# Kernel tuning notes

Hardware: AMD Instinct MI355X
Metric: run time of the kernel (lower is better)

## Reference

```python
import jax, jax.numpy as jnp
import numpy as np
from jax import lax

N_SIN = 3

def _bn(x, g, b, m, v, eps):
    sh = [1] * x.ndim; sh[1] = -1
    r = lambda t: t.reshape(sh)
    return (x - r(m)) / jnp.sqrt(r(v) + eps) * r(g) + r(b)

def _conv2d(x, w, b, padding):
    y = lax.conv_general_dilated(x, w, (1, 1), padding,
                                 dimension_numbers=('NCHW', 'OIHW', 'NCHW'))
    return y + b[None, :, None, None]

def _causal_conv1d(x, w, b):
    k = w.shape[-1]
    y = lax.conv_general_dilated(x, w, (1,), [(k - 1, 0)],
                                 dimension_numbers=('NCH', 'OIH', 'NCH'))
    return y + b[None, :, None]

def _se(x, w1, w2):
    y = x.mean(axis=2)                                   # [B,C] global avg pool
    y = jax.nn.sigmoid(jax.nn.relu(y @ w1.T) @ w2.T)
    return x * y[:, :, None]

def _kan(x, W1, W2, B1, B2):
    # x: [B,din]; per-edge tiny MLP: sin/cos embed -> linear -> silu -> linear
    omega = (2.0 ** jnp.arange(N_SIN)).astype(x.dtype)   # [n_sin]
    ox = x[..., None] * omega                            # [B,din,n_sin]
    feat = jnp.concatenate([x[..., None], jnp.sin(ox), jnp.cos(ox)], axis=-1)  # [B,din,7]
    h = jnp.einsum('bif,ijhf->bijh', feat, W1) + B1[None]  # [B,din,dout,h]
    h = jax.nn.silu(h)
    out = jnp.einsum('bijh,ijh->bij', h, W2[:, :, 0, :]) + B2[None, :, :, 0]
    return out.sum(axis=1)                               # [B,dout]

def _lstm(x, w_ih, w_hh, b_ih, b_hh):
    B, T, E = x.shape
    H = w_hh.shape[1]
    def step(carry, xt):
        h, c = carry
        g = xt @ w_ih.T + h @ w_hh.T + (b_ih + b_hh)
        i, f, gg, o = jnp.split(g, 4, axis=-1)           # torch gate order i,f,g,o
        c = jax.nn.sigmoid(f) * c + jax.nn.sigmoid(i) * jnp.tanh(gg)
        h = jax.nn.sigmoid(o) * jnp.tanh(c)
        return (h, c), h
    init = (jnp.zeros((B, H), x.dtype), jnp.zeros((B, H), x.dtype))
    _, hs = lax.scan(step, init, jnp.swapaxes(x, 0, 1))
    return jnp.swapaxes(hs, 0, 1)                        # [B,T,H]

def _cluster(hidden):
    B, T, H = hidden.shape
    last = hidden[:, -1, :]
    hn = hidden / jnp.maximum(jnp.linalg.norm(hidden, axis=-1, keepdims=True), 1e-8)
    sim = jnp.einsum('bth,bsh->bts', hn, hn)
    sim = jnp.exp(-5.5 * (1.0 - sim))
    sim = sim * (1.0 - jnp.eye(T, dtype=sim.dtype))      # zero diagonal
    # 2-D prefix sums replace the O(T) python loop over block means
    S = jnp.cumsum(jnp.cumsum(sim, axis=1), axis=2)
    Sii = jnp.diagonal(S, axis1=1, axis2=2)[:, :T - 1]   # sum of [:i,:i]
    R = S[:, -1, :T - 1]                                 # sum of [:, :i]
    C = S[:, :T - 1, -1]                                 # sum of [:i, :]
    tot = S[:, -1, -1][:, None]
    i_f = jnp.arange(1, T, dtype=sim.dtype)
    dist = (Sii / i_f**2
            + (tot - R - C + Sii) / (T - i_f)**2
            - (C - Sii) / (i_f * (T - i_f))
            - (R - Sii) / (i_f * (T - i_f)))             # [B,T-1]
    cuts = jnp.argmax(dist, axis=1) + 1                  # [B]
    mask = (jnp.arange(T)[None, :] < cuts[:, None]).astype(hidden.dtype)
    corr = (hidden * mask[:, :, None]).sum(axis=1) / cuts[:, None].astype(hidden.dtype)
    return last, corr

def reference(x, we1, be1, bn_e1_g, bn_e1_b, bn_e1_m, bn_e1_v, we2, be2, bn_e2_g, bn_e2_b, bn_e2_m, bn_e2_v, w_ih, w_hh, b_ih, b_hh, mu_W1, mu_W2, mu_B1, mu_B2, std_W1, std_W2, std_B1, std_B2, muc_W1, muc_W2, muc_B1, muc_B2, stdc_W1, stdc_W2, stdc_B1, stdc_B2, fc_W1, fc_W2, fc_B1, fc_B2, wc1, bc1, bn1_g, bn1_b, bn1_m, bn1_v, se1_w1, se1_w2, wc2, bc2, bn2_g, bn2_b, bn2_m, bn2_v, se2_w1, se2_w2, wc3, bc3, bn3_g, bn3_b, bn3_m, bn3_v, eps1, eps2):
    gelu = lambda t: jax.nn.gelu(t, approximate=False)
    x = jnp.transpose(x, (0, 2, 1))                      # shuffle: [B,T,F]->[B,F,T]
    h2d = _conv2d(x[:, None], we1, be1, 'SAME')          # [B,4E,F,T]
    h2d = gelu(_bn(h2d, bn_e1_g, bn_e1_b, bn_e1_m, bn_e1_v, 1e-5))
    h2d = _conv2d(h2d, we2, be2, 'VALID')                # [B,E,1,T]
    h2d = gelu(_bn(h2d, bn_e2_g, bn_e2_b, bn_e2_m, bn_e2_v, 1e-5))
    x_src = jnp.transpose(h2d[:, :, 0, :], (0, 2, 1))    # [B,T,E]
    hseq = _lstm(x_src, w_ih, w_hh, b_ih, b_hh)          # [B,T,H]
    out, corr = _cluster(hseq)
    mu = _kan(corr, mu_W1, mu_W2, mu_B1, mu_B2)
    std = jax.nn.softplus(_kan(corr, std_W1, std_W2, std_B1, std_B2) - 5.0)
    z = mu + std * eps1
    x_z = jnp.concatenate([out, z], axis=1)              # [B,2H]
    mu_c = _kan(x_z, muc_W1, muc_W2, muc_B1, muc_B2)
    std_c = jax.nn.softplus(_kan(x_z, stdc_W1, stdc_W2, stdc_B1, stdc_B2) - 5.0)
    x1 = mu_c + std_c * eps2                             # dropout = identity (eval)
    x2 = jnp.transpose(x, (0, 2, 1))                     # [B,T,F]: channels = seq_len
    x2 = gelu(_bn(_causal_conv1d(x2, wc1, bc1), bn1_g, bn1_b, bn1_m, bn1_v, 1e-3))
    x2 = _se(x2, se1_w1, se1_w2)
    x2 = gelu(_bn(_causal_conv1d(x2, wc2, bc2), bn2_g, bn2_b, bn2_m, bn2_v, 1e-3))
    x2 = _se(x2, se2_w1, se2_w2)
    x2 = gelu(_bn(_causal_conv1d(x2, wc3, bc3), bn3_g, bn3_b, bn3_m, bn3_v, 1e-3))
    x2 = x2.mean(axis=2)                                 # [B,conv3_nf]
    x_all = jnp.concatenate([x1, x2], axis=1)            # [B, H+conv3_nf]
    return _kan(x_all, fc_W1, fc_W2, fc_B1, fc_B2)       # [B,num_classes]

def setup_inputs():
    key = jax.random.key(0)
    ks = iter(jax.random.split(key, 128))
    f32 = jnp.float32
    def n(shape, s=0.05):
        return s * jax.random.normal(next(ks), shape, f32)
    def bn_params(c):
        g = 1.0 + 0.05 * jax.random.normal(next(ks), (c,), f32)
        b = 0.05 * jax.random.normal(next(ks), (c,), f32)
        m = 0.05 * jax.random.normal(next(ks), (c,), f32)
        v = jax.random.uniform(next(ks), (c,), f32, 0.5, 1.5)
        return g, b, m, v
    def kan_params(din, dout, h=32, feat=1 + 2 * N_SIN):
        s = (2.0 / (feat + h)) ** 0.5
        return (n((din, dout, h, feat), s), n((din, dout, 1, h), s),
                jnp.zeros((din, dout, h), f32), jnp.zeros((din, dout, 1), f32))
    B, T, F_, E, H = 32, 256, 32, 64, 128
    inp = {}
    inp['x'] = jax.random.normal(next(ks), (B, T, F_), f32)
    inp['we1'] = n((4 * E, 1, 1, 8)); inp['be1'] = n((4 * E,))
    inp['bn_e1_g'], inp['bn_e1_b'], inp['bn_e1_m'], inp['bn_e1_v'] = bn_params(4 * E)
    inp['we2'] = n((E, 4 * E, F_, 1)); inp['be2'] = n((E,))
    inp['bn_e2_g'], inp['bn_e2_b'], inp['bn_e2_m'], inp['bn_e2_v'] = bn_params(E)
    inp['w_ih'] = n((4 * H, E)); inp['w_hh'] = n((4 * H, H))
    inp['b_ih'] = n((4 * H,)); inp['b_hh'] = n((4 * H,))
    for nm, (di, do) in [('mu', (H, H)), ('std', (H, H)), ('muc', (2 * H, H)), ('stdc', (2 * H, H)), ('fc', (2 * H, 10))]:
        w1, w2, b1, b2 = kan_params(di, do)
        inp[nm + '_W1'], inp[nm + '_W2'], inp[nm + '_B1'], inp[nm + '_B2'] = w1, w2, b1, b2
    inp['wc1'] = n((128, T, 8)); inp['bc1'] = n((128,))
    inp['bn1_g'], inp['bn1_b'], inp['bn1_m'], inp['bn1_v'] = bn_params(128)
    inp['se1_w1'] = n((8, 128)); inp['se1_w2'] = n((128, 8))
    inp['wc2'] = n((256, 128, 5)); inp['bc2'] = n((256,))
    inp['bn2_g'], inp['bn2_b'], inp['bn2_m'], inp['bn2_v'] = bn_params(256)
    inp['se2_w1'] = n((16, 256)); inp['se2_w2'] = n((256, 16))
    inp['wc3'] = n((128, 256, 3)); inp['bc3'] = n((128,))
    inp['bn3_g'], inp['bn3_b'], inp['bn3_m'], inp['bn3_v'] = bn_params(128)
    inp['eps1'] = jax.random.normal(next(ks), (B, H), f32)
    inp['eps2'] = jax.random.normal(next(ks), (B, H), f32)
    return inp
```

## Files before the change

### kernel.cpp

```cpp
#include <hip/hip_runtime.h>
#include <hip/hip_bf16.h>
#include <math.h>

typedef __hip_bfloat16 bf16;

#define DEV static __device__ __forceinline__

DEV float geluf(float x){ return 0.5f*x*(1.0f + erff(x*0.70710678118654752f)); }
DEV float sigmf(float x){ return 1.0f/(1.0f + __expf(-x)); }
DEV float softplusf(float x){ return (x > 15.f) ? x : log1pf(__expf(x)); }
DEV float tanhfast(float x){ float e = __expf(2.f*x); return fmaf(-2.f, 1.f/(e+1.f), 1.f); }

typedef __attribute__((ext_vector_type(8))) short v8s;
typedef __attribute__((ext_vector_type(4))) float v4f;
typedef _Float16 f16;
typedef f16 h2 __attribute__((ext_vector_type(2)));
typedef f16 f16x8 __attribute__((ext_vector_type(8)));
typedef unsigned u32x4 __attribute__((ext_vector_type(4)));

DEV float dot2f(h2 a, h2 b, float c){
#if __has_builtin(__builtin_amdgcn_fdot2)
  return __builtin_amdgcn_fdot2(a, b, c, false);
#else
  return fmaf((float)a.y, (float)b.y, fmaf((float)a.x, (float)b.x, c));
#endif
}

DEV h2 geth2(f16x8 v, int j){ h2 r; r.x = v[2*j]; r.y = v[2*j+1]; return r; }

DEV void lds_barrier(){
  asm volatile("s_waitcnt lgkmcnt(0)" ::: "memory");
  __builtin_amdgcn_s_barrier();
  __builtin_amdgcn_sched_barrier(0);
}

enum : size_t {
  OFF_W1F   = 0,
  OFF_B1F   = 2048,
  OFF_S2E   = 2304,
  OFF_B2E   = 2368,
  OFF_WIHT  = 2432,
  OFF_BIASG = 35200,
  OFF_WHHT  = 35712,
  OFF_EPI1S = 101248,
  OFF_EPI1B = 101376,
  OFF_EPI2S = 101504,
  OFF_EPI2B = 101760,
  OFF_EPI3S = 102016,
  OFF_EPI3B = 102144,
  OFF_WE2B  = 102272,
  OFF_XSRC  = 364416,
  OFF_GX    = 888704,
  OFF_HSEQ  = 5083008,
  OFF_HN    = 6131584,
  OFF_PCOL  = 7180160,
  OFF_CCOL  = 7188352,
  OFF_CUTS  = 7196544,
  OFF_LAST  = 7196576,
  OFF_CORR  = 7200672,
  OFF_FEATA = 7204768,
  OFF_MUO   = 7233440,
  OFF_STDO  = 7237536,
  OFF_XZ    = 7241632,
  OFF_FEATB = 7249824,
  OFF_MUCO  = 7307168,
  OFF_STDCO = 7311264,
  OFF_XC1   = 7315360,
  OFF_XC2   = 7446432,
  OFF_KP    = 7708576,
  OFF_B2S   = 7741344,
  OFF_X2F   = 7839648,
  OFF_XALL  = 7843744,
  OFF_FEATC = 7851936,
  WS_FLOATS = 7909280
};

__global__ __launch_bounds__(256) void prep_kernel(
    const float* we1, const float* be1,
    const float* e1g, const float* e1b, const float* e1m, const float* e1v,
    const float* we2, const float* be2, const float* e2g, const float* e2b, const float* e2m, const float* e2v,
    const float* wih, const float* whh, const float* bih, const float* bhh,
    const float* bc1, const float* c1g, const float* c1b, const float* c1m, const float* c1v,
    const float* bc2, const float* c2g, const float* c2b, const float* c2m, const float* c2v,
    const float* bc3, const float* c3g, const float* c3b, const float* c3m, const float* c3v,
    const float* muB2, const float* sdB2, const float* mcB2, const float* scB2, const float* fcB2,
    float* ws)
{
  int idx = blockIdx.x*256 + threadIdx.x;
  if(idx < 2048){
    int o = idx>>3;
    float s = e1g[o] * rsqrtf(e1v[o] + 1e-5f);
    ws[OFF_W1F + idx] = we1[idx] * s;
  } else if(idx < 2304){
    int o = idx - 2048;
    float s = e1g[o] * rsqrtf(e1v[o] + 1e-5f);
    ws[OFF_B1F + o] = s*(be1[o] - e1m[o]) + e1b[o];
  } else if(idx < 2368){
    int e = idx - 2304;
    float s = e2g[e] * rsqrtf(e2v[e] + 1e-5f);
    ws[OFF_S2E + e] = s;
    ws[OFF_B2E + e] = s*(be2[e] - e2m[e]) + e2b[e];
  } else if(idx < 35136){
    int q = idx - 2368; int e = q>>9, g = q&511;
    ws[OFF_WIHT + q] = wih[g*64 + e];
  } else if(idx < 35648){
    int g = idx - 35136;
    ws[OFF_BIASG + g] = bih[g] + bhh[g];
  } else if(idx < 101184){
    int q = idx - 35648;
    if(q < 32768){
      int k2 = q>>9, g = q&511;
      h2 v;
      v.x = (f16)whh[g*128 + 2*k2];
      v.y = (f16)whh[g*128 + 2*k2 + 1];
      ((h2*)(ws + OFF_WHHT))[g*64 + k2] = v;
    }
  } else if(idx < 101312){
    int o = idx - 101184;
    float s = c1g[o] * rsqrtf(c1v[o] + 1e-3f);
    ws[OFF_EPI1S + o] = s;
    ws[OFF_EPI1B + o] = s*(bc1[o] - c1m[o]) + c1b[o];
  } else if(idx < 101568){
    int o = idx - 101312;
    float s = c2g[o] * rsqrtf(c2v[o] + 1e-3f);
    ws[OFF_EPI2S + o] = s;
    ws[OFF_EPI2B + o] = s*(bc2[o] - c2m[o]) + c2b[o];
  } else if(idx < 101696){
    int o = idx - 101568;
    float s = c3g[o] * rsqrtf(c3v[o] + 1e-3f);
    ws[OFF_EPI3S + o] = s;
    ws[OFF_EPI3B + o] = s*(bc3[o] - c3m[o]) + c3b[o];
  } else if(idx < 625984){
    int q = idx - 101696;
    int o = q >> 11, rem = q & 2047;
    int e = rem >> 5, f = rem & 31;
    bf16* Wr = (bf16*)(ws + OFF_WE2B);
    Wr[q] = __float2bfloat16(we2[(size_t)e*8192 + o*32 + f]);
  } else if(idx < 626112){
    int j = idx - 625984; float s = 0.f;
    for(int i=0;i<128;i++) s += muB2[i*128+j];
    ws[OFF_B2S + j] = s;
  } else if(idx < 626240){
    int j = idx - 626112; float s = 0.f;
    for(int i=0;i<128;i++) s += sdB2[i*128+j];
    ws[OFF_B2S + 128 + j] = s;
  } else if(idx < 626368){
    int j = idx - 626240; float s = 0.f;
    for(int i=0;i<256;i++) s += mcB2[i*128+j];
    ws[OFF_B2S + 256 + j] = s;
  } else if(idx < 626496){
    int j = idx - 626368; float s = 0.f;
    for(int i=0;i<256;i++) s += scB2[i*128+j];
    ws[OFF_B2S + 384 + j] = s;
  } else if(idx < 626506){
    int j = idx - 626496; float s = 0.f;
    for(int i=0;i<256;i++) s += fcB2[i*10+j];
    ws[OFF_B2S + 512 + j] = s;
  }
}

__global__ __launch_bounds__(256,1) void encoder_kernel(
    const float* __restrict__ x, const float* __restrict__ w1f, const float* __restrict__ b1f,
    const float* __restrict__ s2e, const float* __restrict__ b2e,
    const bf16* __restrict__ Wr, float* __restrict__ x_src)
{
  __shared__ float xs[39*32];
  __shared__ float w1s[2048];
  __shared__ float b1s[256];
  __shared__ __align__(16) unsigned short At[2][32*136];
  __shared__ __align__(16) unsigned short Bt[2][4*2560];

  int blk = blockIdx.x; int b = blk>>3; int t0 = (blk&7)*32;
  int tid = threadIdx.x;

  for(int i=tid;i<2048;i+=256) w1s[i] = w1f[i];
  b1s[tid] = b1f[tid];
  for(int i=tid;i<39*32;i+=256){
    int r=i>>5, f=i&31; int t=t0-3+r;
    xs[i] = (t>=0 && t<256) ? x[(b*256+t)*32+f] : 0.f;
  }
  __syncthreads();

  int f = tid & 31, tq = tid >> 5;
  int lane = tid & 63, w = tid >> 6;
  int wm = w & 1, wn = w >> 1;
  int m0 = wm*16, n0 = wn*32;
  int l15 = lane & 15, quad = lane >> 4;

  const v8s* Wv = (const v8s*)Wr;

  auto stage = [&](int cc, int buf){
    v8s bw[4];
    #pragma unroll
    for(int i=0;i<4;i++) bw[i] = Wv[cc*1024 + i*256 + tid];
    unsigned short aval[16];
    #pragma unroll
    for(int ol=0;ol<4;ol++){
      int o = cc*4 + ol;
      float wv[8];
      #pragma unroll
      for(int j=0;j<8;j++) wv[j] = w1s[o*8+j];
      float bb = b1s[o];
      #pragma unroll
      for(int i=0;i<4;i++){
        int tl = tq*4 + i;
        float c = bb;
        #pragma unroll
        for(int j=0;j<8;j++) c = fmaf(wv[j], xs[(tl+j)*32+f], c);
        aval[ol*4+i] = ((__hip_bfloat16_raw)__float2bfloat16(geluf(c))).x;
      }
    }
    #pragma unroll
    for(int ol=0;ol<4;ol++){
      #pragma unroll
      for(int i=0;i<4;i++)
        At[buf][(tq*4+i)*136 + ol*32 + f] = aval[ol*4+i];
    }
    #pragma unroll
    for(int i=0;i<4;i++){
      int j = i*256 + tid;
      int ol = j>>8, e = (j&255)>>2, f8 = j&3;
      *(v8s*)&Bt[buf][ol*2560 + e*40 + f8*8] = bw[i];
    }
  };

  stage(0, 0);
  __syncthreads();

  v4f acc0 = {0.f,0.f,0.f,0.f}, acc1 = {0.f,0.f,0.f,0.f};

  for(int c=0;c<64;c++){
    int p = c & 1, q = p ^ 1;
    if(c < 63) stage(c+1, q);
    #pragma unroll
    for(int ol=0;ol<4;ol++){
      v8s av = *(const v8s*)&At[p][(m0+l15)*136 + ol*32 + quad*8];
      v8s b0 = *(const v8s*)&Bt[p][ol*2560 + (n0+l15)*40 + quad*8];
      v8s b1 = *(const v8s*)&Bt[p][ol*2560 + (n0+16+l15)*40 + quad*8];
      acc0 = __builtin_amdgcn_mfma_f32_16x16x32_bf16(av, b0, acc0, 0, 0, 0);
      acc1 = __builtin_amdgcn_mfma_f32_16x16x32_bf16(av, b1, acc1, 0, 0, 0);
    }
    __syncthreads();
  }

  #pragma unroll
  for(int r=0;r<4;r++){
    int t = t0 + m0 + quad*4 + r;
    int e0 = n0 + l15;
    float v0 = geluf(s2e[e0]*acc0[r] + b2e[e0]);
    x_src[((size_t)(b*256+t))*64 + e0] = v0;
    int e1 = e0 + 16;
    float v1 = geluf(s2e[e1]*acc1[r] + b2e[e1]);
    x_src[((size_t)(b*256+t))*64 + e1] = v1;
  }
}

__global__ __launch_bounds__(256) void gates_kernel(
    const float* x_src, const float* wihT, const float* biasg, float* gx)
{
  __shared__ float xsh[32*64];
  int blk = blockIdx.x; int b = blk>>3, t0 = (blk&7)*32;
  int tid = threadIdx.x;
  for(int i=tid;i<2048;i+=256) xsh[i] = x_src[((size_t)b*256+t0)*64 + i];
  __syncthreads();
  int g0 = tid, g1 = tid + 256;
  float acc0[32], acc1[32];
  #pragma unroll
  for(int tt=0;tt<32;tt++){ acc0[tt]=0.f; acc1[tt]=0.f; }
  for(int e=0;e<64;e++){
    float w0 = wihT[e*512+g0], w1 = wihT[e*512+g1];
    #pragma unroll
    for(int tt=0;tt<32;tt++){
      float xv = xsh[tt*64+e];
      acc0[tt] = fmaf(xv, w0, acc0[tt]);
      acc1[tt] = fmaf(xv, w1, acc1[tt]);
    }
  }
  float bg0 = biasg[g0], bg1 = biasg[g1];
  #pragma unroll
  for(int tt=0;tt<32;tt++){
    gx[((size_t)b*256+t0+tt)*512 + g0] = acc0[tt] + bg0;
    gx[((size_t)b*256+t0+tt)*512 + g1] = acc1[tt] + bg1;
  }
}

#define LSTM_STEP(AG, BG, PR, PW, T)                                         \
  {                                                                          \
    const f16x8* hp = (const f16x8*)&hsh[PR][half*64];                       \
    f16x8 hvv[8];                                                            \
    _Pragma("unroll")                                                        \
    for(int q=0;q<8;q++) hvv[q] = hp[q];                                     \
    float sA0=0.f,sA1=0.f,sB0=0.f,sB1=0.f;                                   \
    _Pragma("unroll")                                                        \
    for(int q=0;q<8;q++){                                                    \
      f16x8 W8a = __builtin_bit_cast(f16x8, wa[q]);                          \
      f16x8 W8b = __builtin_bit_cast(f16x8, wb[q]);                          \
      f16x8 hq = hvv[q];                                                     \
      sA0 = dot2f(geth2(hq,0), geth2(W8a,0), sA0);                           \
      sA1 = dot2f(geth2(hq,1), geth2(W8a,1), sA1);                           \
      sA0 = dot2f(geth2(hq,2), geth2(W8a,2), sA0);                           \
      sA1 = dot2f(geth2(hq,3), geth2(W8a,3), sA1);                           \
      sB0 = dot2f(geth2(hq,0), geth2(W8b,0), sB0);                           \
      sB1 = dot2f(geth2(hq,1), geth2(W8b,1), sB1);                           \
      sB0 = dot2f(geth2(hq,2), geth2(W8b,2), sB0);                           \
      sB1 = dot2f(geth2(hq,3), geth2(W8b,3), sB1);                           \
    }                                                                        \
    float pA = sA0+sA1, pB = sB0+sB1;                                        \
    float fullA = (AG) + pA + __shfl_xor(pA, 32, 64);                        \
    float fullB = (BG) + pB + __shfl_xor(pB, 32, 64);                        \
    float argA = dup ? 2.f*fullA : -fullA;                                   \
    float eA = __expf(argA);                                                 \
    float qA = 1.f/(eA + 1.f);                                               \
    float vA = dup ? fmaf(-2.f, qA, 1.f) : qA;      \
    float vB = 1.f/(1.f + __expf(-fullB));          \
    float oA = __shfl_xor(vA, 16, 64);                                       \
    float oB = __shfl_xor(vB, 16, 64);                                       \
    float iv = dup ? oA : vA;                                                \
    float gv = dup ? vA : oA;                                                \
    float fv = dup ? oB : vB;                                                \
    float ov = dup ? vB : oB;                                                \
    c = fmaf(fv, c, iv*gv);                                                  \
    float h = ov*tanhfast(c);                                                \
    if(lane < 16){                                                           \
      hsh[PW][n] = (f16)h;                                                   \
      hseq[((size_t)b*256+(T))*128 + n] = h;                                 \
    }                                                                        \
    lds_barrier();                                                           \
  }

__global__ __launch_bounds__(512)
__attribute__((amdgpu_waves_per_eu(2,2)))
void lstm_kernel(
    const float* __restrict__ gates_x, const float* __restrict__ whh16f, float* __restrict__ hseq)
{
  __shared__ __align__(16) f16 hsh[2][128];
  int b = blockIdx.x, tt = threadIdx.x;
  int wave = tt >> 6, lane = tt & 63;
  int n = wave*16 + (lane & 15);
  int dup  = (lane >> 4) & 1;
  int half = lane >> 5;
  int gA = dup ? (256 + n) : n;
  int gB = gA + 128;

  const u32x4* Wp = (const u32x4*)whh16f;
  u32x4 wa[8], wb[8];
  #pragma unroll
  for(int q=0;q<8;q++){
    wa[q] = Wp[gA*16 + half*8 + q];
    wb[q] = Wp[gB*16 + half*8 + q];
  }
  asm volatile("" :
    "+v"(wa[0]), "+v"(wa[1]), "+v"(wa[2]), "+v"(wa[3]),
    "+v"(wa[4]), "+v"(wa[5]), "+v"(wa[6]), "+v"(wa[7]),
    "+v"(wb[0]), "+v"(wb[1]), "+v"(wb[2]), "+v"(wb[3]),
    "+v"(wb[4]), "+v"(wb[5]), "+v"(wb[6]), "+v"(wb[7]));

  if(tt < 128) hsh[0][tt] = (f16)0.f;
  float c = 0.f;
  const float* gx = gates_x + (size_t)b*256*512;
  float aC = gx[gA],       bC = gx[gB];
  float aN = gx[512 + gA], bN = gx[512 + gB];
  __syncthreads();
  for(int t=0; t<256; t+=2){
    float a2=0.f, b2=0.f, a3=0.f, b3=0.f;
    if(t+2 < 256){ a2 = gx[(size_t)(t+2)*512 + gA]; b2 = gx[(size_t)(t+2)*512 + gB]; }
    LSTM_STEP(aC, bC, 0, 1, t);
    if(t+3 < 256){ a3 = gx[(size_t)(t+3)*512 + gA]; b3 = gx[(size_t)(t+3)*512 + gB]; }
    LSTM_STEP(aN, bN, 1, 0, t+1);
    aC=a2; bC=b2; aN=a3; bN=b3;
  }
}

__global__ __launch_bounds__(64) void hn_kernel(const float* hseq, float* hn)
{
  size_t row = blockIdx.x; int lane = threadIdx.x;
  const float* hp = hseq + row*128;
  float v0 = hp[lane], v1 = hp[lane+64];
  float ss = v0*v0 + v1*v1;
  #pragma unroll
  for(int m=1;m<64;m<<=1) ss += __shfl_xor(ss, m, 64);
  float r = 1.f / fmaxf(sqrtf(ss), 1e-8f);
  hn[row*128 + lane]      = v0*r;
  hn[row*128 + 64 + lane] = v1*r;
}

__global__ __launch_bounds__(256) void pc_kernel(const float* hn, float* pcol, float* ccol)
{
  int blk = blockIdx.x; int b = blk>>3, chunk = blk&7;
  int tid = threadIdx.x; int il = tid & 31, ts = tid >> 5;
  int i = chunk*32 + il;
  const float4* hb = (const float4*)(hn + (size_t)b*32768);
  float4 hi[32];
  #pragma unroll
  for(int r=0;r<32;r++) hi[r] = hb[(size_t)i*32 + r];
  float ps=0.f, cs=0.f;
  for(int t=ts*32; t<ts*32+32; t++){
    float dx=0.f, dy=0.f, dz=0.f, dw=0.f;
    #pragma unroll
    for(int r=0;r<32;r++){
      float4 hv = hb[(size_t)t*32 + r];
      dx = fmaf(hi[r].x, hv.x, dx);
      dy = fmaf(hi[r].y, hv.y, dy);
      dz = fmaf(hi[r].z, hv.z, dz);
      dw = fmaf(hi[r].w, hv.w, dw);
    }
    float dot = (dx+dy)+(dz+dw);
    float sim = (t==i) ? 0.f : expf(-5.5f*(1.0f - dot));
    cs += sim;
    if(t < i) ps += sim;
  }
  __shared__ float red[16][32];
  red[ts][il] = ps; red[8+ts][il] = cs;
  __syncthreads();
  if(tid < 32){
    float s=0.f;
    for(int r=0;r<8;r++) s += red[r][tid];
    pcol[b*256 + chunk*32 + tid] = s;
  } else if(tid < 64){
    int c2 = tid - 32; float s=0.f;
    for(int r=0;r<8;r++) s += red[8+r][c2];
    ccol[b*256 + chunk*32 + c2] = s;
  }
}

__global__ __launch_bounds__(256) void cutcorr_kernel(
    const float* pcol, const float* ccol, const float* hseq,
    float* last, float* corr, int* cuts)
{
  int b = blockIdx.x, tid = threadIdx.x;
  __shared__ float D[256], RC[256], dist[256];
  __shared__ int cutsh;
  if(tid == 0){
    float d=0.f, r=0.f;
    for(int i=0;i<256;i++){
      d += 2.f*pcol[b*256+i]; D[i]=d;
      r += ccol[b*256+i];     RC[i]=r;
    }
  }
  __syncthreads();
  float tot = RC[255];
  if(tid < 255){
    float Dv = D[tid], Rv = RC[tid];
    float i_f = (float)(tid+1), j_f = 256.f - i_f;
    dist[tid] = Dv/(i_f*i_f) + (tot - 2.f*Rv + Dv)/(j_f*j_f) - 2.f*(Rv - Dv)/(i_f*j_f);
  }
  __syncthreads();
  if(tid == 0){
    float best = dist[0]; int bi = 0;
    for(int i=1;i<255;i++) if(dist[i] > best){ best = dist[i]; bi = i; }
    cutsh = bi + 1; cuts[b] = cutsh;
  }
  __syncthreads();
  int cut = cutsh;
  int k = tid & 127, half = tid >> 7;
  float s = 0.f;
  for(int t=half; t<cut; t+=2) s += hseq[((size_t)b*256+t)*128 + k];
  __shared__ float partial[2][128];
  partial[half][k] = s;
  __syncthreads();
  if(tid < 128){
    corr[b*128+tid] = (partial[0][tid] + partial[1][tid]) / (float)cut;
    last[b*128+tid] = hseq[((size_t)b*256+255)*128 + tid];
  }
}

__global__ __launch_bounds__(256) void feat_kernel(const float* xin, float* feat, int n)
{
  int idx = blockIdx.x*256 + threadIdx.x;
  if(idx >= n) return;
  float xv = xin[idx];
  float* fp = feat + (size_t)idx*7;
  fp[0]=xv;
  fp[1]=sinf(xv); fp[2]=sinf(2.f*xv); fp[3]=sinf(4.f*xv);
  fp[4]=cosf(xv); fp[5]=cosf(2.f*xv); fp[6]=cosf(4.f*xv);
}

__global__ __launch_bounds__(256) void kanp_kernel(
    const float* __restrict__ feat, const float* __restrict__ W1,
    const float* __restrict__ B1, const float* __restrict__ W2,
    int din, int dout, float* __restrict__ partial)
{
  __shared__ float feat_s[32*225];
  __shared__ float red[8][32];
  int j = blockIdx.x, ic = blockIdx.y;
  int i0 = ic*32;
  int tid = threadIdx.x;
  int b = tid & 31, hg = tid >> 5;
  for(int q=tid; q<1792; q+=256){
    int br = q/56, qq = q - br*56;
    float4 v = *(const float4*)(feat + ((size_t)br*din + i0)*7 + qq*4);
    float* d = &feat_s[br*225 + qq*4];
    d[0]=v.x; d[1]=v.y; d[2]=v.z; d[3]=v.w;
  }
  __syncthreads();
  float acc = 0.f;
  const float* fb = &feat_s[b*225];
  for(int ii=0; ii<32; ii++){
    int i = i0 + ii;
    size_t hbase = ((size_t)i*dout + j)*32 + hg*4;
    const float4* w1p = (const float4*)(W1 + ((size_t)i*dout + j)*224 + hg*28);
    float w1a[28];
    #pragma unroll
    for(int q=0;q<7;q++) *(float4*)&w1a[q*4] = w1p[q];
    float4 b1v = *(const float4*)(B1 + hbase);
    float4 w2v = *(const float4*)(W2 + hbase);
    float f[7];
    #pragma unroll
    for(int q=0;q<7;q++) f[q] = fb[ii*7+q];
    float b1a[4] = {b1v.x, b1v.y, b1v.z, b1v.w};
    float w2a[4] = {w2v.x, w2v.y, w2v.z, w2v.w};
    #pragma unroll
    for(int hh=0;hh<4;hh++){
      float hv = b1a[hh];
      #pragma unroll
      for(int q=0;q<7;q++) hv = fmaf(f[q], w1a[hh*7+q], hv);
      float sv = hv / (1.f + __expf(-hv));
      acc = fmaf(sv, w2a[hh], acc);
    }
  }
  red[hg][b] = acc;
  __syncthreads();
  if(tid < 32){
    float s = 0.f;
    #pragma unroll
    for(int q=0;q<8;q++) s += red[q][tid];
    partial[((size_t)ic*32 + tid)*dout + j] = s;
  }
}

__global__ __launch_bounds__(256) void kanr_kernel(
    const float* __restrict__ partial, const float* __restrict__ b2s,
    int NI, int dout, float* __restrict__ outp)
{
  int idx = blockIdx.x*256 + threadIdx.x;
  if(idx >= 32*dout) return;
  int b = idx / dout, j = idx - b*dout;
  float s = b2s[j];
  for(int ic=0; ic<NI; ic++) s += partial[((size_t)ic*32 + b)*dout + j];
  outp[idx] = s;
}

__global__ __launch_bounds__(256) void zmix_kernel(
    const float* muo, const float* stdo, const float* eps1, const float* last, float* xz)
{
  int idx = blockIdx.x*256 + threadIdx.x;
  if(idx >= 4096) return;
  int b = idx >> 7, k = idx & 127;
  float z = muo[idx] + softplusf(stdo[idx] - 5.f)*eps1[idx];
  xz[b*256 + k]       = last[idx];
  xz[b*256 + 128 + k] = z;
}

__global__ __launch_bounds__(256) void xall_kernel(
    const float* muco, const float* stdco, const float* eps2, const float* x2f, float* xa)
{
  int idx = blockIdx.x*256 + threadIdx.x;
  if(idx >= 4096) return;
  int b = idx >> 7, k = idx & 127;
  xa[b*256 + k]       = muco[idx] + softplusf(stdco[idx] - 5.f)*eps2[idx];
  xa[b*256 + 128 + k] = x2f[idx];
}

template<int CIN, int K, int COUT, int NCH, int LG>
__global__ __launch_bounds__(COUT*LG, 1) void convp_kernel(
    const float* __restrict__ xin, const float* __restrict__ w, float* __restrict__ part)
{
  constexpr int L = 32/LG;
  constexpr int CCH = CIN/NCH;
  __shared__ float xsh[CCH*32];
  int b = blockIdx.x, ch = blockIdx.y;
  int tid = threadIdx.x;
  for(int i=tid; i<CCH*32; i+=COUT*LG) xsh[i] = xin[((size_t)b*CIN + ch*CCH)*32 + i];
  __syncthreads();
  int o = tid / LG, lh = tid % LG;
  int l0 = lh*L;
  float acc[L];
  #pragma unroll
  for(int j=0;j<L;j++) acc[j]=0.f;
  const float* wrow = w + ((size_t)o*CIN + ch*CCH)*K;
  for(int c=0;c<CCH;c++){
    float wv[K];
    #pragma unroll
    for(int k=0;k<K;k++) wv[k] = wrow[c*K + k];
    float xr[L+K-1];
    #pragma unroll
    for(int i=0;i<L+K-1;i++){
      int li = l0 - (K-1) + i;
      xr[i] = (li>=0) ? xsh[c*32+li] : 0.f;
    }
    #pragma unroll
    for(int j=0;j<L;j++){
      #pragma unroll
      for(int k=0;k<K;k++) acc[j] = fmaf(xr[j+k], wv[k], acc[j]);
    }
  }
  float* pp = part + (((size_t)ch*32 + b)*COUT + o)*32 + l0;
  #pragma unroll
  for(int j=0;j<L;j++) pp[j] = acc[j];
}

template<int C, int R, int NP>
__global__ __launch_bounds__(C,1) void sef_kernel(
    const float* __restrict__ part, const float* __restrict__ epi_s, const float* __restrict__ epi_b,
    const float* __restrict__ w1, const float* __restrict__ w2, float* __restrict__ out)
{
  __shared__ float mean[C];
  __shared__ float y1[R];
  int b = blockIdx.x, c = threadIdx.x;
  float g[32];
  #pragma unroll
  for(int l=0;l<32;l++) g[l]=0.f;
  for(int p=0;p<NP;p++){
    const float* pp = part + (((size_t)p*32 + b)*C + c)*32;
    #pragma unroll
    for(int l=0;l<32;l++) g[l] += pp[l];
  }
  float s = epi_s[c], bb = epi_b[c];
  float m = 0.f;
  #pragma unroll
  for(int l=0;l<32;l++){ g[l] = geluf(s*g[l]+bb); m += g[l]; }
  mean[c] = m*(1.f/32.f);
  __syncthreads();
  if(c < R){
    float t=0.f;
    for(int k=0;k<C;k++) t = fmaf(mean[k], w1[c*C+k], t);
    y1[c] = fmaxf(t,0.f);
  }
  __syncthreads();
  float t=0.f;
  #pragma unroll
  for(int k=0;k<R;k++) t = fmaf(y1[k], w2[c*R+k], t);
  float sc = sigmf(t);
  float* op = out + ((size_t)b*C + c)*32;
  #pragma unroll
  for(int l=0;l<32;l++) op[l] = g[l]*sc;
}

__global__ __launch_bounds__(128,1) void mean3f_kernel(
    const float* __restrict__ part, const float* __restrict__ epi_s, const float* __restrict__ epi_b,
    float* __restrict__ x2f)
{
  int b = blockIdx.x, c = threadIdx.x;
  float g[32];
  #pragma unroll
  for(int l=0;l<32;l++) g[l]=0.f;
  for(int p=0;p<8;p++){
    const float* pp = part + (((size_t)p*32 + b)*128 + c)*32;
    #pragma unroll
    for(int l=0;l<32;l++) g[l] += pp[l];
  }
  float s = epi_s[c], bb = epi_b[c];
  float m = 0.f;
  #pragma unroll
  for(int l=0;l<32;l++) m += geluf(s*g[l]+bb);
  x2f[b*128 + c] = m*(1.f/32.f);
}

extern "C" void kernel_launch(void* const* d_in, const int* in_sizes, int n_in,
                              void* d_out, int out_size, void* d_ws, size_t ws_size,
                              hipStream_t stream)
{
  const float* x    = (const float*)d_in[0];
  const float* we1  = (const float*)d_in[1];
  const float* be1  = (const float*)d_in[2];
  const float* e1g  = (const float*)d_in[3];
  const float* e1b  = (const float*)d_in[4];
  const float* e1m  = (const float*)d_in[5];
  const float* e1v  = (const float*)d_in[6];
  const float* we2  = (const float*)d_in[7];
  const float* be2  = (const float*)d_in[8];
  const float* e2g  = (const float*)d_in[9];
  const float* e2b  = (const float*)d_in[10];
  const float* e2m  = (const float*)d_in[11];
  const float* e2v  = (const float*)d_in[12];
  const float* wih  = (const float*)d_in[13];
  const float* whh  = (const float*)d_in[14];
  const float* bih  = (const float*)d_in[15];
  const float* bhh  = (const float*)d_in[16];
  const float* muW1 = (const float*)d_in[17];
  const float* muW2 = (const float*)d_in[18];
  const float* muB1 = (const float*)d_in[19];
  const float* muB2 = (const float*)d_in[20];
  const float* sdW1 = (const float*)d_in[21];
  const float* sdW2 = (const float*)d_in[22];
  const float* sdB1 = (const float*)d_in[23];
  const float* sdB2 = (const float*)d_in[24];
  const float* mcW1 = (const float*)d_in[25];
  const float* mcW2 = (const float*)d_in[26];
  const float* mcB1 = (const float*)d_in[27];
  const float* mcB2 = (const float*)d_in[28];
  const float* scW1 = (const float*)d_in[29];
  const float* scW2 = (const float*)d_in[30];
  const float* scB1 = (const float*)d_in[31];
  const float* scB2 = (const float*)d_in[32];
  const float* fcW1 = (const float*)d_in[33];
  const float* fcW2 = (const float*)d_in[34];
  const float* fcB1 = (const float*)d_in[35];
  const float* fcB2 = (const float*)d_in[36];
  const float* wc1  = (const float*)d_in[37];
  const float* bc1  = (const float*)d_in[38];
  const float* c1g  = (const float*)d_in[39];
  const float* c1b  = (const float*)d_in[40];
  const float* c1m  = (const float*)d_in[41];
  const float* c1v  = (const float*)d_in[42];
  const float* se1w1= (const float*)d_in[43];
  const float* se1w2= (const float*)d_in[44];
  const float* wc2  = (const float*)d_in[45];
  const float* bc2  = (const float*)d_in[46];
  const float* c2g  = (const float*)d_in[47];
  const float* c2b  = (const float*)d_in[48];
  const float* c2m  = (const float*)d_in[49];
  const float* c2v  = (const float*)d_in[50];
  const float* se2w1= (const float*)d_in[51];
  const float* se2w2= (const float*)d_in[52];
  const float* wc3  = (const float*)d_in[53];
  const float* bc3  = (const float*)d_in[54];
  const float* c3g  = (const float*)d_in[55];
  const float* c3b  = (const float*)d_in[56];
  const float* c3m  = (const float*)d_in[57];
  const float* c3v  = (const float*)d_in[58];
  const float* eps1 = (const float*)d_in[59];
  const float* eps2 = (const float*)d_in[60];

  float* ws = (float*)d_ws;
  float* part = ws + OFF_GX;
  float* kp   = ws + OFF_KP;
  float* b2s  = ws + OFF_B2S;

  prep_kernel<<<2448, 256, 0, stream>>>(we1, be1, e1g,e1b,e1m,e1v,
      we2, be2,e2g,e2b,e2m,e2v, wih,whh,bih,bhh,
      bc1,c1g,c1b,c1m,c1v, bc2,c2g,c2b,c2m,c2v, bc3,c3g,c3b,c3m,c3v,
      muB2, sdB2, mcB2, scB2, fcB2, ws);

  encoder_kernel<<<256, 256, 0, stream>>>(x, ws+OFF_W1F, ws+OFF_B1F,
      ws+OFF_S2E, ws+OFF_B2E, (const bf16*)(ws+OFF_WE2B), ws+OFF_XSRC);

  gates_kernel<<<256, 256, 0, stream>>>(ws+OFF_XSRC, ws+OFF_WIHT, ws+OFF_BIASG, ws+OFF_GX);
  lstm_kernel<<<32, 512, 0, stream>>>(ws+OFF_GX, ws+OFF_WHHT, ws+OFF_HSEQ);

  hn_kernel<<<8192, 64, 0, stream>>>(ws+OFF_HSEQ, ws+OFF_HN);
  pc_kernel<<<256, 256, 0, stream>>>(ws+OFF_HN, ws+OFF_PCOL, ws+OFF_CCOL);
  cutcorr_kernel<<<32, 256, 0, stream>>>(ws+OFF_PCOL, ws+OFF_CCOL, ws+OFF_HSEQ,
      ws+OFF_LAST, ws+OFF_CORR, (int*)(ws+OFF_CUTS));

  feat_kernel<<<16, 256, 0, stream>>>(ws+OFF_CORR, ws+OFF_FEATA, 4096);
  kanp_kernel<<<dim3(128,4), 256, 0, stream>>>(ws+OFF_FEATA, muW1, muB1, muW2, 128, 128, kp);
  kanr_kernel<<<16, 256, 0, stream>>>(kp, b2s+0, 4, 128, ws+OFF_MUO);
  kanp_kernel<<<dim3(128,4), 256, 0, stream>>>(ws+OFF_FEATA, sdW1, sdB1, sdW2, 128, 128, kp);
  kanr_kernel<<<16, 256, 0, stream>>>(kp, b2s+128, 4, 128, ws+OFF_STDO);
  zmix_kernel<<<16, 256, 0, stream>>>(ws+OFF_MUO, ws+OFF_STDO, eps1, ws+OFF_LAST, ws+OFF_XZ);
  feat_kernel<<<32, 256, 0, stream>>>(ws+OFF_XZ, ws+OFF_FEATB, 8192);
  kanp_kernel<<<dim3(128,8), 256, 0, stream>>>(ws+OFF_FEATB, mcW1, mcB1, mcW2, 256, 128, kp);
  kanr_kernel<<<16, 256, 0, stream>>>(kp, b2s+256, 8, 128, ws+OFF_MUCO);
  kanp_kernel<<<dim3(128,8), 256, 0, stream>>>(ws+OFF_FEATB, scW1, scB1, scW2, 256, 128, kp);
  kanr_kernel<<<16, 256, 0, stream>>>(kp, b2s+384, 8, 128, ws+OFF_STDCO);

  convp_kernel<256,8,128,8,2><<<dim3(32,8), 256, 0, stream>>>(x, wc1, part);
  sef_kernel<128,8,8><<<32, 128, 0, stream>>>(part, ws+OFF_EPI1S, ws+OFF_EPI1B, se1w1, se1w2, ws+OFF_XC1);
  convp_kernel<128,5,256,4,1><<<dim3(32,4), 256, 0, stream>>>(ws+OFF_XC1, wc2, part);
  sef_kernel<256,16,4><<<32, 256, 0, stream>>>(part, ws+OFF_EPI2S, ws+OFF_EPI2B, se2w1, se2w2, ws+OFF_XC2);
  convp_kernel<256,3,128,8,2><<<dim3(32,8), 256, 0, stream>>>(ws+OFF_XC2, wc3, part);
  mean3f_kernel<<<32, 128, 0, stream>>>(part, ws+OFF_EPI3S, ws+OFF_EPI3B, ws+OFF_X2F);

  xall_kernel<<<16, 256, 0, stream>>>(ws+OFF_MUCO, ws+OFF_STDCO, eps2, ws+OFF_X2F, ws+OFF_XALL);
  feat_kernel<<<32, 256, 0, stream>>>(ws+OFF_XALL, ws+OFF_FEATC, 8192);
  kanp_kernel<<<dim3(10,8), 256, 0, stream>>>(ws+OFF_FEATC, fcW1, fcB1, fcW2, 256, 10, kp);
  kanr_kernel<<<2, 256, 0, stream>>>(kp, b2s+512, 8, 10, (float*)d_out);
}
```

Before: 976.2 us.

## Compute all four LSTM gates per thread with 256-thread blocks

```diff
diff --git a/kernel.cpp b/kernel.cpp
--- a/kernel.cpp
+++ b/kernel.cpp
@@ -284,90 +284,97 @@
   }
 }
 
-#define LSTM_STEP(AG, BG, PR, PW, T)                                         \
+#define LSTM_STEP(GI, GF, GG, GO, PR, PW, T)                                 \
   {                                                                          \
     const f16x8* hp = (const f16x8*)&hsh[PR][half*64];                       \
     f16x8 hvv[8];                                                            \
     _Pragma("unroll")                                                        \
     for(int q=0;q<8;q++) hvv[q] = hp[q];                                     \
-    float sA0=0.f,sA1=0.f,sB0=0.f,sB1=0.f;                                   \
+    float si=0.f, sf=0.f, sg=0.f, so=0.f;                                    \
     _Pragma("unroll")                                                        \
     for(int q=0;q<8;q++){                                                    \
-      f16x8 W8a = __builtin_bit_cast(f16x8, wa[q]);                          \
-      f16x8 W8b = __builtin_bit_cast(f16x8, wb[q]);                          \
+      f16x8 Wi = __builtin_bit_cast(f16x8, wi[q]);                           \
+      f16x8 Wf = __builtin_bit_cast(f16x8, wf[q]);                           \
+      f16x8 Wg = __builtin_bit_cast(f16x8, wg[q]);                           \
+      f16x8 Wo = __builtin_bit_cast(f16x8, wo[q]);                           \
       f16x8 hq = hvv[q];                                                     \
-      sA0 = dot2f(geth2(hq,0), geth2(W8a,0), sA0);                           \
-      sA1 = dot2f(geth2(hq,1), geth2(W8a,1), sA1);                           \
-      sA0 = dot2f(geth2(hq,2), geth2(W8a,2), sA0);                           \
-      sA1 = dot2f(geth2(hq,3), geth2(W8a,3), sA1);                           \
-      sB0 = dot2f(geth2(hq,0), geth2(W8b,0), sB0);                           \
-      sB1 = dot2f(geth2(hq,1), geth2(W8b,1), sB1);                           \
-      sB0 = dot2f(geth2(hq,2), geth2(W8b,2), sB0);                           \
-      sB1 = dot2f(geth2(hq,3), geth2(W8b,3), sB1);                           \
+      _Pragma("unroll")                                                      \
+      for(int j=0;j<4;j++){                                                  \
+        h2 hj = geth2(hq, j);                                                \
+        si = dot2f(hj, geth2(Wi,j), si);                                     \
+        sf = dot2f(hj, geth2(Wf,j), sf);                                     \
+        sg = dot2f(hj, geth2(Wg,j), sg);                                     \
+        so = dot2f(hj, geth2(Wo,j), so);                                     \
+      }                                                                      \
     }                                                                        \
-    float pA = sA0+sA1, pB = sB0+sB1;                                        \
-    float fullA = (AG) + pA + __shfl_xor(pA, 32, 64);                        \
-    float fullB = (BG) + pB + __shfl_xor(pB, 32, 64);                        \
-    float argA = dup ? 2.f*fullA : -fullA;                                   \
-    float eA = __expf(argA);                                                 \
-    float qA = 1.f/(eA + 1.f);                                               \
-    float vA = dup ? fmaf(-2.f, qA, 1.f) : qA;      \
-    float vB = 1.f/(1.f + __expf(-fullB));          \
-    float oA = __shfl_xor(vA, 16, 64);                                       \
-    float oB = __shfl_xor(vB, 16, 64);                                       \
-    float iv = dup ? oA : vA;                                                \
-    float gv = dup ? vA : oA;                                                \
-    float fv = dup ? oB : vB;                                                \
-    float ov = dup ? vB : oB;                                                \
+    si += __shfl_xor(si, 32, 64);                                            \
+    sf += __shfl_xor(sf, 32, 64);                                            \
+    sg += __shfl_xor(sg, 32, 64);                                            \
+    so += __shfl_xor(so, 32, 64);                                            \
+    float iv = sigmf(si + (GI));                                             \
+    float fv = sigmf(sf + (GF));                                             \
+    float gv = tanhfast(sg + (GG));                                          \
+    float ov = sigmf(so + (GO));                                             \
     c = fmaf(fv, c, iv*gv);                                                  \
     float h = ov*tanhfast(c);                                                \
-    if(lane < 16){                                                           \
+    if(half == 0){                                                           \
       hsh[PW][n] = (f16)h;                                                   \
       hseq[((size_t)b*256+(T))*128 + n] = h;                                 \
     }                                                                        \
     lds_barrier();                                                           \
   }
 
-__global__ __launch_bounds__(512)
-__attribute__((amdgpu_waves_per_eu(2,2)))
+__global__ __launch_bounds__(256)
+__attribute__((amdgpu_waves_per_eu(1,1)))
 void lstm_kernel(
     const float* __restrict__ gates_x, const float* __restrict__ whh16f, float* __restrict__ hseq)
 {
   __shared__ __align__(16) f16 hsh[2][128];
   int b = blockIdx.x, tt = threadIdx.x;
   int wave = tt >> 6, lane = tt & 63;
-  int n = wave*16 + (lane & 15);
-  int dup  = (lane >> 4) & 1;
   int half = lane >> 5;
-  int gA = dup ? (256 + n) : n;
-  int gB = gA + 128;
+  int n = wave*32 + (lane & 31);
 
   const u32x4* Wp = (const u32x4*)whh16f;
-  u32x4 wa[8], wb[8];
+  u32x4 wi[8], wf[8], wg[8], wo[8];
   #pragma unroll
   for(int q=0;q<8;q++){
-    wa[q] = Wp[gA*16 + half*8 + q];
-    wb[q] = Wp[gB*16 + half*8 + q];
+    wi[q] = Wp[(size_t)(n      )*16 + half*8 + q];
+    wf[q] = Wp[(size_t)(n + 128)*16 + half*8 + q];
+    wg[q] = Wp[(size_t)(n + 256)*16 + half*8 + q];
+    wo[q] = Wp[(size_t)(n + 384)*16 + half*8 + q];
   }
   asm volatile("" :
-    "+v"(wa[0]), "+v"(wa[1]), "+v"(wa[2]), "+v"(wa[3]),
-    "+v"(wa[4]), "+v"(wa[5]), "+v"(wa[6]), "+v"(wa[7]),
-    "+v"(wb[0]), "+v"(wb[1]), "+v"(wb[2]), "+v"(wb[3]),
-    "+v"(wb[4]), "+v"(wb[5]), "+v"(wb[6]), "+v"(wb[7]));
+    "+v"(wi[0]), "+v"(wi[1]), "+v"(wi[2]), "+v"(wi[3]),
+    "+v"(wi[4]), "+v"(wi[5]), "+v"(wi[6]), "+v"(wi[7]),
+    "+v"(wf[0]), "+v"(wf[1]), "+v"(wf[2]), "+v"(wf[3]),
+    "+v"(wf[4]), "+v"(wf[5]), "+v"(wf[6]), "+v"(wf[7]));
+  asm volatile("" :
+    "+v"(wg[0]), "+v"(wg[1]), "+v"(wg[2]), "+v"(wg[3]),
+    "+v"(wg[4]), "+v"(wg[5]), "+v"(wg[6]), "+v"(wg[7]),
+    "+v"(wo[0]), "+v"(wo[1]), "+v"(wo[2]), "+v"(wo[3]),
+    "+v"(wo[4]), "+v"(wo[5]), "+v"(wo[6]), "+v"(wo[7]));
 
   if(tt < 128) hsh[0][tt] = (f16)0.f;
   float c = 0.f;
   const float* gx = gates_x + (size_t)b*256*512;
-  float aC = gx[gA],       bC = gx[gB];
-  float aN = gx[512 + gA], bN = gx[512 + gB];
+  float i0v = gx[n], f0v = gx[128+n], g0v = gx[256+n], o0v = gx[384+n];
+  float i1v = gx[512+n], f1v = gx[512+128+n], g1v = gx[512+256+n], o1v = gx[512+384+n];
   __syncthreads();
   for(int t=0; t<256; t+=2){
-    float a2=0.f, b2=0.f, a3=0.f, b3=0.f;
-    if(t+2 < 256){ a2 = gx[(size_t)(t+2)*512 + gA]; b2 = gx[(size_t)(t+2)*512 + gB]; }
-    LSTM_STEP(aC, bC, 0, 1, t);
-    if(t+3 < 256){ a3 = gx[(size_t)(t+3)*512 + gA]; b3 = gx[(size_t)(t+3)*512 + gB]; }
-    LSTM_STEP(aN, bN, 1, 0, t+1);
-    aC=a2; bC=b2; aN=a3; bN=b3;
+    float i2v=0.f,f2v=0.f,g2v=0.f,o2v=0.f,i3v=0.f,f3v=0.f,g3v=0.f,o3v=0.f;
+    if(t+2 < 256){
+      const float* gp = gx + (size_t)(t+2)*512;
+      i2v = gp[n]; f2v = gp[128+n]; g2v = gp[256+n]; o2v = gp[384+n];
+    }
+    LSTM_STEP(i0v, f0v, g0v, o0v, 0, 1, t);
+    if(t+3 < 256){
+      const float* gp = gx + (size_t)(t+3)*512;
+      i3v = gp[n]; f3v = gp[128+n]; g3v = gp[256+n]; o3v = gp[384+n];
+    }
+    LSTM_STEP(i1v, f1v, g1v, o1v, 1, 0, t+1);
+    i0v=i2v; f0v=f2v; g0v=g2v; o0v=o2v;
+    i1v=i3v; f1v=f3v; g1v=g3v; o1v=o3v;
   }
 }
 
@@ -736,7 +743,7 @@
       ws+OFF_S2E, ws+OFF_B2E, (const bf16*)(ws+OFF_WE2B), ws+OFF_XSRC);
 
   gates_kernel<<<256, 256, 0, stream>>>(ws+OFF_XSRC, ws+OFF_WIHT, ws+OFF_BIASG, ws+OFF_GX);
-  lstm_kernel<<<32, 512, 0, stream>>>(ws+OFF_GX, ws+OFF_WHHT, ws+OFF_HSEQ);
+  lstm_kernel<<<32, 256, 0, stream>>>(ws+OFF_GX, ws+OFF_WHHT, ws+OFF_HSEQ);
 
   hn_kernel<<<8192, 64, 0, stream>>>(ws+OFF_HSEQ, ws+OFF_HN);
   pc_kernel<<<256, 256, 0, stream>>>(ws+OFF_HN, ws+OFF_PCOL, ws+OFF_CCOL);
```

After: 966.7 us. No clear change (-1.0%).
